# Optimization experiments

Hardware: AMD Instinct MI355X
Metric: run time of the kernel (lower is better)

## Reference

```python
import jax, jax.numpy as jnp
import numpy as np

COMMITMENT_COST = 0.25


def setup_inputs() -> dict:
    key = jax.random.key(0)
    k1, k2 = jax.random.split(key)
    inputs = jax.random.normal(k1, (32, 64, 64, 64), dtype=jnp.float32)  # BCHW, C=embedding_dim
    codebook = jax.random.normal(k2, (1024, 64), dtype=jnp.float32)      # [n_embeddings, embedding_dim]
    return {"inputs": inputs, "codebook": codebook}


def reference(inputs, codebook):
    B, C, H, W = inputs.shape
    K, D = codebook.shape  # D == C
    x = jnp.transpose(inputs, (0, 2, 3, 1))          # BHWC
    flat = x.reshape(-1, D)                          # [N, D]
    # squared-euclidean distances [N, K]
    distances = (jnp.sum(flat * flat, axis=1, keepdims=True)
                 + jnp.sum(codebook * codebook, axis=1)
                 - 2.0 * flat @ codebook.T)
    logits = -distances
    idx = jnp.argmax(logits, axis=-1)                # [N]
    oh = jax.nn.one_hot(idx, K, dtype=flat.dtype)    # [N, K]
    # straight-through one-hot
    oh_st = oh + logits - jax.lax.stop_gradient(logits)
    oh_encodings = jnp.transpose(oh_st.reshape(B, H * W, K), (0, 2, 1))  # b d n
    # quantized computed under no_grad in torch -> full stop_gradient
    quantized = jax.lax.stop_gradient(oh_st @ codebook).reshape(x.shape)  # BHWC
    e_latent_loss = jnp.mean((quantized - x) ** 2)
    loss = COMMITMENT_COST * e_latent_loss
    q_st = x + jax.lax.stop_gradient(quantized - x)  # straight-through output
    avg_probs = jnp.mean(oh_st, axis=0)              # [K]
    perplexity = jnp.exp(-jnp.sum(avg_probs * jnp.log(avg_probs + 1e-10)))
    return (loss, jnp.transpose(q_st, (0, 3, 1, 2)), perplexity, oh_encodings)
```

## Files before the change

### kernel.cpp

```cpp
#include <hip/hip_runtime.h>
#include <math.h>

typedef _Float16 half8 __attribute__((ext_vector_type(8)));
typedef float f32x4 __attribute__((ext_vector_type(4)));
typedef float f32x2 __attribute__((ext_vector_type(2)));

#define NBLK     1024
#define Q_OFF    1
#define PERP_OFF 8388609
#define OH_OFF   8388610
#define LOSS_N   8388608.0f

#define CB2_OFF_B 16384
#define IDX_OFF_W 69632

__global__ __launch_bounds__(256) void k0_prep(const float* __restrict__ cb,
                                               float* __restrict__ cnorm,
                                               int* __restrict__ hist,
                                               char* __restrict__ cb2) {
  int k = blockIdx.x * 256 + threadIdx.x;
  hist[k] = 0;
  const float* row = cb + (size_t)k * 64;
  const float4* r4 = (const float4*)row;
  float s = 0.f;
#pragma unroll
  for (int i = 0; i < 16; ++i) {
    float4 v = r4[i];
    s += v.x * v.x + v.y * v.y + v.z * v.z + v.w * v.w;
  }
  cnorm[k] = s;

  int tile = k >> 4, c = k & 15;
  char* base = cb2 + tile * 4096;
#pragma unroll
  for (int d16 = 0; d16 < 8; ++d16) {
    half8 hh, ll;
#pragma unroll
    for (int i = 0; i < 8; ++i) {
      float v = row[d16 * 8 + i];
      _Float16 h = (_Float16)v;
      hh[i] = h;
      ll[i] = (_Float16)(v - (float)h);
    }
    int off = (d16 >> 2) * 1024 + c * 64 + (d16 & 3) * 16;
    *(half8*)(base + off) = hh;
    *(half8*)(base + 2048 + off) = ll;
  }
}

__global__ __launch_bounds__(256, 4) void k1_main(
    const float* __restrict__ in, const float* __restrict__ cb,
    const char* __restrict__ cb2, const float* __restrict__ cnorm,
    int* __restrict__ hist, float* __restrict__ partial,
    int* __restrict__ idx, float* __restrict__ out) {
  __shared__ int bestk_s[128];
  __shared__ float red[256];

  const int tid = threadIdx.x;
  const int bid = blockIdx.x;
  const int w = tid >> 6, l = tid & 63, q = l & 15, g = l >> 4;
  const int b = bid >> 5;
  const int hw0 = (bid & 31) << 7;

  half8 ah[2][2], al[2][2];
  {
    const float* xb = in + ((size_t)b << 18);
#pragma unroll
    for (int a = 0; a < 2; ++a) {
      const int hw = hw0 + w * 32 + a * 16 + q;
#pragma unroll
      for (int ks = 0; ks < 2; ++ks) {
#pragma unroll
        for (int i = 0; i < 8; ++i) {
          float v = xb[((size_t)(ks * 32 + g * 8 + i) << 12) + hw];
          _Float16 h = (_Float16)v;
          ah[a][ks][i] = h;
          al[a][ks][i] = (_Float16)(v - (float)h);
        }
      }
    }
  }

  float bd0[4], bd1[4];
  int bk0[4], bk1[4];
#pragma unroll
  for (int j = 0; j < 4; ++j) { bd0[j] = bd1[j] = 3.4e38f; bk0[j] = bk1[j] = 0; }

  const int boff = q * 64 + g * 16;
  f32x2* ohz = (f32x2*)(out + OH_OFF);
  const f32x2 z2 = {0.f, 0.f};
  const size_t slab = (size_t)bid * 65536 + tid;

  for (int tb = 0; tb < 64; ++tb) {
    const char* tbase = cb2 + tb * 4096 + boff;
    half8 bh0 = *(const half8*)(tbase);
    half8 bh1 = *(const half8*)(tbase + 1024);
    half8 bl0 = *(const half8*)(tbase + 2048);
    half8 bl1 = *(const half8*)(tbase + 3072);
    const int code = tb * 16 + q;
    const float cn = cnorm[code];
    const f32x4 z = {0.f, 0.f, 0.f, 0.f};
    f32x4 s = __builtin_amdgcn_mfma_f32_16x16x32_f16(ah[0][0], bh0, z, 0, 0, 0);
    s = __builtin_amdgcn_mfma_f32_16x16x32_f16(al[0][0], bh0, s, 0, 0, 0);
    s = __builtin_amdgcn_mfma_f32_16x16x32_f16(ah[0][0], bl0, s, 0, 0, 0);
    f32x4 t = __builtin_amdgcn_mfma_f32_16x16x32_f16(ah[0][1], bh1, z, 0, 0, 0);
    t = __builtin_amdgcn_mfma_f32_16x16x32_f16(al[0][1], bh1, t, 0, 0, 0);
    t = __builtin_amdgcn_mfma_f32_16x16x32_f16(ah[0][1], bl1, t, 0, 0, 0);
    s = s + t;
#pragma unroll
    for (int j = 0; j < 4; ++j) {
      float d = fmaf(-2.f, s[j], cn);
      if (d < bd0[j]) { bd0[j] = d; bk0[j] = code; }
    }
    f32x4 u = __builtin_amdgcn_mfma_f32_16x16x32_f16(ah[1][0], bh0, z, 0, 0, 0);
    u = __builtin_amdgcn_mfma_f32_16x16x32_f16(al[1][0], bh0, u, 0, 0, 0);
    u = __builtin_amdgcn_mfma_f32_16x16x32_f16(ah[1][0], bl0, u, 0, 0, 0);
    f32x4 v = __builtin_amdgcn_mfma_f32_16x16x32_f16(ah[1][1], bh1, z, 0, 0, 0);
    v = __builtin_amdgcn_mfma_f32_16x16x32_f16(al[1][1], bh1, v, 0, 0, 0);
    v = __builtin_amdgcn_mfma_f32_16x16x32_f16(ah[1][1], bl1, v, 0, 0, 0);
    u = u + v;
#pragma unroll
    for (int j = 0; j < 4; ++j) {
      float d = fmaf(-2.f, u[j], cn);
      if (d < bd1[j]) { bd1[j] = d; bk1[j] = code; }
    }
    {
      size_t zb = slab + (size_t)tb * 1024;
#pragma unroll
      for (int r = 0; r < 4; ++r)
        __builtin_nontemporal_store(z2, &ohz[zb + r * 256]);
    }
  }

#pragma unroll
  for (int m = 1; m < 16; m <<= 1) {
#pragma unroll
    for (int j = 0; j < 4; ++j) {
      float od = __shfl_xor(bd0[j], m, 64);
      int ok = __shfl_xor(bk0[j], m, 64);
      if (od < bd0[j] || (od == bd0[j] && ok < bk0[j])) { bd0[j] = od; bk0[j] = ok; }
      od = __shfl_xor(bd1[j], m, 64);
      ok = __shfl_xor(bk1[j], m, 64);
      if (od < bd1[j] || (od == bd1[j] && ok < bk1[j])) { bd1[j] = od; bk1[j] = ok; }
    }
  }
  if (q == 0) {
#pragma unroll
    for (int j = 0; j < 4; ++j) {
      bestk_s[w * 32 + g * 4 + j] = bk0[j];
      bestk_s[w * 32 + 16 + g * 4 + j] = bk1[j];
    }
  }
  __syncthreads();

  const int p = tid & 127, hf = tid >> 7;
  const int kq = bestk_s[p];
  if (hf == 0) {
    idx[bid * 128 + p] = kq;
    atomicAdd(&hist[kq], 1);
  }
  float lsum = 0.f;
  {
    const float* xb = in + ((size_t)b << 18) + hw0 + p;
    float* yb = out + Q_OFF + ((size_t)b << 18) + hw0 + p;
    const float* qrow = cb + (size_t)kq * 64;
#pragma unroll
    for (int c = 0; c < 32; ++c) {
      const int cc = hf * 32 + c;
      float x = xb[(size_t)cc << 12];
      float f = qrow[cc] - x;
      lsum += f * f;
      yb[(size_t)cc << 12] = x + f;
    }
  }
  red[tid] = lsum;
  __syncthreads();
#pragma unroll
  for (int sft = 128; sft > 0; sft >>= 1) {
    if (tid < sft) red[tid] += red[tid + sft];
    __syncthreads();
  }
  if (tid == 0) partial[bid] = red[0];
}

__global__ __launch_bounds__(1024) void k2_finalize(const int* __restrict__ hist,
                                                    const float* __restrict__ partial,
                                                    float* __restrict__ out) {
  __shared__ float red[1024];
  int tid = threadIdx.x;

  red[tid] = partial[tid];
  __syncthreads();
  for (int s = 512; s > 0; s >>= 1) {
    if (tid < s) red[tid] += red[tid + s];
    __syncthreads();
  }
  if (tid == 0) out[0] = 0.25f * (red[0] / LOSS_N);
  __syncthreads();

  float pr = (float)hist[tid] * (1.0f / 131072.0f);
  red[tid] = pr * logf(pr + 1e-10f);
  __syncthreads();
  for (int s = 512; s > 0; s >>= 1) {
    if (tid < s) red[tid] += red[tid + s];
    __syncthreads();
  }
  if (tid == 0) out[PERP_OFF] = expf(-red[0]);
}

__global__ __launch_bounds__(256) void k3_scatter(const int* __restrict__ idx,
                                                  float* __restrict__ out) {
  int n = blockIdx.x * 256 + threadIdx.x;
  int k = idx[n];
  int b = n >> 12;
  int pos = n & 4095;
  out[OH_OFF + ((((size_t)b << 10) + (size_t)k) << 12) + pos] = 1.0f;
}

extern "C" void kernel_launch(void* const* d_in, const int* in_sizes, int n_in,
                              void* d_out, int out_size, void* d_ws, size_t ws_size,
                              hipStream_t stream) {
  const float* in = (const float*)d_in[0];
  const float* cb = (const float*)d_in[1];
  float* out = (float*)d_out;

  float* cnorm   = (float*)d_ws;
  int*   hist    = (int*)d_ws + 1024;
  float* partial = (float*)d_ws + 2048;
  char*  cb2b    = (char*)d_ws + CB2_OFF_B;
  int*   idx     = (int*)d_ws + IDX_OFF_W;

  k0_prep<<<4, 256, 0, stream>>>(cb, cnorm, hist, cb2b);
  k1_main<<<NBLK, 256, 0, stream>>>(in, cb, cb2b, cnorm, hist, partial, idx, out);
  k2_finalize<<<1, 1024, 0, stream>>>(hist, partial, out);
  k3_scatter<<<512, 256, 0, stream>>>(idx, out);
}
```

Before: 224.9 us.

## Split one-hot zero-fill into dedicated blocks interleaved with compute blocks

```diff
diff --git a/kernel.cpp b/kernel.cpp
--- a/kernel.cpp
+++ b/kernel.cpp
@@ -3,13 +3,14 @@
 
 typedef _Float16 half8 __attribute__((ext_vector_type(8)));
 typedef float f32x4 __attribute__((ext_vector_type(4)));
-typedef float f32x2 __attribute__((ext_vector_type(2)));
-
-#define NBLK     1024
+
+#define NBLK_TOT 1536
 #define Q_OFF    1
 #define PERP_OFF 8388609
 #define OH_OFF   8388610
 #define LOSS_N   8388608.0f
+#define OH_F4_BASE 8388612
+#define OH_NF4     33554431
 
 #define CB2_OFF_B 16384
 #define IDX_OFF_W 69632
@@ -58,9 +59,35 @@
 
   const int tid = threadIdx.x;
   const int bid = blockIdx.x;
+  const int r3 = bid % 3;
+
+  if (r3 == 2) {
+    const int fi = bid / 3;
+    float4* base = (float4*)(out + OH_F4_BASE);
+    const float4 z4 = make_float4(0.f, 0.f, 0.f, 0.f);
+    const size_t b0 = (size_t)fi * 65536 + tid;
+    if (fi < 511) {
+#pragma unroll 8
+      for (int i = 0; i < 256; ++i) base[b0 + (size_t)i * 256] = z4;
+    } else {
+#pragma unroll 8
+      for (int i = 0; i < 256; ++i) {
+        size_t i4 = b0 + (size_t)i * 256;
+        if (i4 < OH_NF4) base[i4] = z4;
+      }
+      if (tid == 0) {
+        out[OH_OFF] = 0.f; out[OH_OFF + 1] = 0.f;
+        out[OH_F4_BASE + 4 * (size_t)OH_NF4] = 0.f;
+        out[OH_F4_BASE + 4 * (size_t)OH_NF4 + 1] = 0.f;
+      }
+    }
+    return;
+  }
+
+  const int ci = (bid / 3) * 2 + r3;
+  const int b = ci >> 5;
+  const int hw0 = (ci & 31) << 7;
   const int w = tid >> 6, l = tid & 63, q = l & 15, g = l >> 4;
-  const int b = bid >> 5;
-  const int hw0 = (bid & 31) << 7;
 
   half8 ah[2][2], al[2][2];
   {
@@ -87,9 +114,6 @@
   for (int j = 0; j < 4; ++j) { bd0[j] = bd1[j] = 3.4e38f; bk0[j] = bk1[j] = 0; }
 
   const int boff = q * 64 + g * 16;
-  f32x2* ohz = (f32x2*)(out + OH_OFF);
-  const f32x2 z2 = {0.f, 0.f};
-  const size_t slab = (size_t)bid * 65536 + tid;
 
   for (int tb = 0; tb < 64; ++tb) {
     const char* tbase = cb2 + tb * 4096 + boff;
@@ -124,12 +148,6 @@
       float d = fmaf(-2.f, u[j], cn);
       if (d < bd1[j]) { bd1[j] = d; bk1[j] = code; }
     }
-    {
-      size_t zb = slab + (size_t)tb * 1024;
-#pragma unroll
-      for (int r = 0; r < 4; ++r)
-        __builtin_nontemporal_store(z2, &ohz[zb + r * 256]);
-    }
   }
 
 #pragma unroll
@@ -156,7 +174,7 @@
   const int p = tid & 127, hf = tid >> 7;
   const int kq = bestk_s[p];
   if (hf == 0) {
-    idx[bid * 128 + p] = kq;
+    idx[ci * 128 + p] = kq;
     atomicAdd(&hist[kq], 1);
   }
   float lsum = 0.f;
@@ -180,7 +198,7 @@
     if (tid < sft) red[tid] += red[tid + sft];
     __syncthreads();
   }
-  if (tid == 0) partial[bid] = red[0];
+  if (tid == 0) partial[ci] = red[0];
 }
 
 __global__ __launch_bounds__(1024) void k2_finalize(const int* __restrict__ hist,
@@ -231,7 +249,7 @@
   int*   idx     = (int*)d_ws + IDX_OFF_W;
 
   k0_prep<<<4, 256, 0, stream>>>(cb, cnorm, hist, cb2b);
-  k1_main<<<NBLK, 256, 0, stream>>>(in, cb, cb2b, cnorm, hist, partial, idx, out);
+  k1_main<<<NBLK_TOT, 256, 0, stream>>>(in, cb, cb2b, cnorm, hist, partial, idx, out);
   k2_finalize<<<1, 1024, 0, stream>>>(hist, partial, out);
   k3_scatter<<<512, 256, 0, stream>>>(idx, out);
 }
```

Result: no change. 223.0 us (-0.9%).

## Split one-hot zero-fill into dedicated blocks and merge finalize with scatter

Applied to the files above, without the earlier changes.

```diff
diff --git a/kernel.cpp b/kernel.cpp
--- a/kernel.cpp
+++ b/kernel.cpp
@@ -5,7 +5,6 @@
 typedef float f32x4 __attribute__((ext_vector_type(4)));
 typedef float f32x2 __attribute__((ext_vector_type(2)));
 
-#define NBLK     1024
 #define Q_OFF    1
 #define PERP_OFF 8388609
 #define OH_OFF   8388610
@@ -58,9 +57,20 @@
 
   const int tid = threadIdx.x;
   const int bid = blockIdx.x;
+  const int rank = bid >> 1;
+
+  if (((bid ^ (bid >> 3)) & 1) == 0) {
+    f32x2* dst = (f32x2*)(out + OH_OFF) + (size_t)rank * 65536 + tid;
+    const f32x2 z2 = {0.f, 0.f};
+#pragma unroll 8
+    for (int i = 0; i < 256; ++i) dst[(size_t)i * 256] = z2;
+    return;
+  }
+
+  const int ci = rank;
+  const int b = ci >> 5;
+  const int hw0 = (ci & 31) << 7;
   const int w = tid >> 6, l = tid & 63, q = l & 15, g = l >> 4;
-  const int b = bid >> 5;
-  const int hw0 = (bid & 31) << 7;
 
   half8 ah[2][2], al[2][2];
   {
@@ -87,9 +97,6 @@
   for (int j = 0; j < 4; ++j) { bd0[j] = bd1[j] = 3.4e38f; bk0[j] = bk1[j] = 0; }
 
   const int boff = q * 64 + g * 16;
-  f32x2* ohz = (f32x2*)(out + OH_OFF);
-  const f32x2 z2 = {0.f, 0.f};
-  const size_t slab = (size_t)bid * 65536 + tid;
 
   for (int tb = 0; tb < 64; ++tb) {
     const char* tbase = cb2 + tb * 4096 + boff;
@@ -124,12 +131,6 @@
       float d = fmaf(-2.f, u[j], cn);
       if (d < bd1[j]) { bd1[j] = d; bk1[j] = code; }
     }
-    {
-      size_t zb = slab + (size_t)tb * 1024;
-#pragma unroll
-      for (int r = 0; r < 4; ++r)
-        __builtin_nontemporal_store(z2, &ohz[zb + r * 256]);
-    }
   }
 
 #pragma unroll
@@ -156,7 +157,7 @@
   const int p = tid & 127, hf = tid >> 7;
   const int kq = bestk_s[p];
   if (hf == 0) {
-    idx[bid * 128 + p] = kq;
+    idx[ci * 128 + p] = kq;
     atomicAdd(&hist[kq], 1);
   }
   float lsum = 0.f;
@@ -180,41 +181,52 @@
     if (tid < sft) red[tid] += red[tid + sft];
     __syncthreads();
   }
-  if (tid == 0) partial[bid] = red[0];
-}
-
-__global__ __launch_bounds__(1024) void k2_finalize(const int* __restrict__ hist,
-                                                    const float* __restrict__ partial,
-                                                    float* __restrict__ out) {
-  __shared__ float red[1024];
-  int tid = threadIdx.x;
-
-  red[tid] = partial[tid];
-  __syncthreads();
-  for (int s = 512; s > 0; s >>= 1) {
-    if (tid < s) red[tid] += red[tid + s];
+  if (tid == 0) partial[ci] = red[0];
+}
+
+__global__ __launch_bounds__(256) void k_final(const int* __restrict__ idx,
+                                               const int* __restrict__ hist,
+                                               const float* __restrict__ partial,
+                                               float* __restrict__ out) {
+  const int tid = threadIdx.x;
+  const int bid = blockIdx.x;
+  if (bid < 512) {
+    int n = bid * 256 + tid;
+    int k = idx[n];
+    int b = n >> 12;
+    int pos = n & 4095;
+    out[OH_OFF + ((((size_t)b << 10) + (size_t)k) << 12) + pos] = 1.0f;
+    return;
+  }
+
+  __shared__ float red[256];
+  float s = (partial[tid] + partial[tid + 512]) +
+            (partial[tid + 256] + partial[tid + 768]);
+  red[tid] = s;
+  __syncthreads();
+#pragma unroll
+  for (int st = 128; st > 0; st >>= 1) {
+    if (tid < st) red[tid] += red[tid + st];
     __syncthreads();
   }
   if (tid == 0) out[0] = 0.25f * (red[0] / LOSS_N);
   __syncthreads();
 
-  float pr = (float)hist[tid] * (1.0f / 131072.0f);
-  red[tid] = pr * logf(pr + 1e-10f);
-  __syncthreads();
-  for (int s = 512; s > 0; s >>= 1) {
-    if (tid < s) red[tid] += red[tid + s];
+  const float invn = 1.0f / 131072.0f;
+  float p0 = (float)hist[tid] * invn;
+  float p1 = (float)hist[tid + 256] * invn;
+  float p2 = (float)hist[tid + 512] * invn;
+  float p3 = (float)hist[tid + 768] * invn;
+  float e = (p0 * logf(p0 + 1e-10f) + p2 * logf(p2 + 1e-10f)) +
+            (p1 * logf(p1 + 1e-10f) + p3 * logf(p3 + 1e-10f));
+  red[tid] = e;
+  __syncthreads();
+#pragma unroll
+  for (int st = 128; st > 0; st >>= 1) {
+    if (tid < st) red[tid] += red[tid + st];
     __syncthreads();
   }
   if (tid == 0) out[PERP_OFF] = expf(-red[0]);
-}
-
-__global__ __launch_bounds__(256) void k3_scatter(const int* __restrict__ idx,
-                                                  float* __restrict__ out) {
-  int n = blockIdx.x * 256 + threadIdx.x;
-  int k = idx[n];
-  int b = n >> 12;
-  int pos = n & 4095;
-  out[OH_OFF + ((((size_t)b << 10) + (size_t)k) << 12) + pos] = 1.0f;
 }
 
 extern "C" void kernel_launch(void* const* d_in, const int* in_sizes, int n_in,
@@ -231,7 +243,6 @@
   int*   idx     = (int*)d_ws + IDX_OFF_W;
 
   k0_prep<<<4, 256, 0, stream>>>(cb, cnorm, hist, cb2b);
-  k1_main<<<NBLK, 256, 0, stream>>>(in, cb, cb2b, cnorm, hist, partial, idx, out);
-  k2_finalize<<<1, 1024, 0, stream>>>(hist, partial, out);
-  k3_scatter<<<512, 256, 0, stream>>>(idx, out);
-}
+  k1_main<<<2048, 256, 0, stream>>>(in, cb, cb2b, cnorm, hist, partial, idx, out);
+  k_final<<<513, 256, 0, stream>>>(idx, hist, partial, out);
+}
```

Result: slower. 280.0 us (+24.5%).
